# Performance work log

Hardware: AMD Instinct MI355X
Metric: run time of the kernel (lower is better)

Reference implementation:

```python
import jax, jax.numpy as jnp
import numpy as np

B, K, D_MODEL = 64, 256, 512
D_STATE, D_CONV, EXPAND = 16, 4, 1
D_INNER = EXPAND * D_MODEL
DT_RANK = (D_MODEL + 15) // 16  # 32
EPS = 1e-5


def _layer_norm(x, g, b):
    m = jnp.mean(x, axis=-1, keepdims=True)
    v = jnp.mean(jnp.square(x - m), axis=-1, keepdims=True)
    return (x - m) * jax.lax.rsqrt(v + EPS) * g + b


def _silu(x):
    return x * jax.nn.sigmoid(x)


def _mamba_block(x, in_proj_w, conv_w, conv_b, x_proj_w, dt_proj_w, dt_proj_b, A_log, Dp, out_proj_w):
    # x: (B, K, d_model)
    b, k, _ = x.shape
    d_inner = A_log.shape[0]
    d_state = A_log.shape[1]
    dt_rank = dt_proj_w.shape[1]
    xz = x @ in_proj_w.T                      # (B, K, 2*d_inner)
    xi, z = jnp.split(xz, 2, axis=-1)
    # causal depthwise conv1d, width d_conv
    pad = conv_w.shape[1] - 1
    xp = jnp.pad(xi, ((0, 0), (pad, 0), (0, 0)))
    xc = conv_b + sum(xp[:, w:w + k, :] * conv_w[:, w] for w in range(conv_w.shape[1]))
    xc = _silu(xc)
    proj = xc @ x_proj_w.T                    # (B, K, dt_rank + 2*d_state)
    dtr = proj[..., :dt_rank]
    Bc = proj[..., dt_rank:dt_rank + d_state]  # (B, K, d_state)
    Cc = proj[..., dt_rank + d_state:]         # (B, K, d_state)
    dt = jax.nn.softplus(dtr @ dt_proj_w.T + dt_proj_b)  # (B, K, d_inner)
    A = -jnp.exp(A_log)                       # (d_inner, d_state)

    def step(h, inp):
        dt_t, x_t, B_t, C_t = inp             # (B,d_inner),(B,d_inner),(B,d_state),(B,d_state)
        dA = jnp.exp(dt_t[:, :, None] * A)    # (B, d_inner, d_state)
        h = dA * h + (dt_t * x_t)[:, :, None] * B_t[:, None, :]
        y = jnp.einsum('bds,bs->bd', h, C_t)
        return h, y

    h0 = jnp.zeros((b, d_inner, d_state), x.dtype)
    xs = (dt.transpose(1, 0, 2), xc.transpose(1, 0, 2),
          Bc.transpose(1, 0, 2), Cc.transpose(1, 0, 2))
    _, ys = jax.lax.scan(step, h0, xs)        # ys: (K, B, d_inner)
    y = ys.transpose(1, 0, 2) + xc * Dp       # skip term D*x
    y = y * _silu(z)
    return y @ out_proj_w.T


def setup_inputs() -> dict:
    key = jax.random.key(0)
    ks = jax.random.split(key, 8)
    s = 0.02
    slots = jax.random.normal(ks[0], (B, K, D_MODEL), dtype=jnp.float32)
    in_proj_w = jax.random.normal(ks[1], (2 * D_INNER, D_MODEL), jnp.float32) * s
    conv_w = jax.random.normal(ks[2], (D_INNER, D_CONV), jnp.float32) * 0.1
    conv_b = jnp.zeros((D_INNER,), jnp.float32)
    x_proj_w = jax.random.normal(ks[3], (DT_RANK + 2 * D_STATE, D_INNER), jnp.float32) * s
    dt_proj_w = jax.random.normal(ks[4], (D_INNER, DT_RANK), jnp.float32) * s
    dt_proj_b = jax.random.normal(ks[5], (D_INNER,), jnp.float32) * 0.1 - 4.0  # small softplus(dt)
    A_log = jnp.log(jnp.broadcast_to(jnp.arange(1, D_STATE + 1, dtype=jnp.float32), (D_INNER, D_STATE)))
    Dp = jnp.ones((D_INNER,), jnp.float32)
    out_proj_w = jax.random.normal(ks[6], (D_MODEL, D_INNER), jnp.float32) * s
    ln_g = jnp.ones((D_MODEL,), jnp.float32)
    ln_b = jnp.zeros((D_MODEL,), jnp.float32)
    fln_g = jnp.ones((D_MODEL,), jnp.float32)
    fln_b = jnp.zeros((D_MODEL,), jnp.float32)
    return {"slots": slots, "ln_g": ln_g, "ln_b": ln_b,
            "in_proj_w": in_proj_w, "conv_w": conv_w, "conv_b": conv_b,
            "x_proj_w": x_proj_w, "dt_proj_w": dt_proj_w, "dt_proj_b": dt_proj_b,
            "A_log": A_log, "Dp": Dp, "out_proj_w": out_proj_w,
            "fln_g": fln_g, "fln_b": fln_b}


def reference(slots, ln_g, ln_b, in_proj_w, conv_w, conv_b, x_proj_w,
              dt_proj_w, dt_proj_b, A_log, Dp, out_proj_w, fln_g, fln_b):
    x = slots
    # num_layers = 1: pre-norm -> mamba -> residual
    residual = x
    x = _layer_norm(x, ln_g, ln_b)
    x = _mamba_block(x, in_proj_w, conv_w, conv_b, x_proj_w,
                     dt_proj_w, dt_proj_b, A_log, Dp, out_proj_w)
    x = x + residual
    return _layer_norm(x, fln_g, fln_b)
```

## Files before the change

kernel.cpp:

```cpp
#include <hip/hip_runtime.h>
#include <hip/hip_bf16.h>


#define NTOK 16384
#define DM   512

typedef __attribute__((ext_vector_type(8))) short bf16x8;
typedef __attribute__((ext_vector_type(4))) float f32x4;

__device__ __forceinline__ unsigned short f2bf(float f){
  unsigned int u = __float_as_uint(f);
  u = (u + 0x7fffu + ((u >> 16) & 1u)) >> 16;
  return (unsigned short)u;
}
__device__ __forceinline__ float bfu(unsigned short p){ return __uint_as_float(((unsigned int)p) << 16); }
__device__ __forceinline__ unsigned int pk2(float a, float b){
  return (unsigned int)f2bf(a) | ((unsigned int)f2bf(b) << 16);
}
__device__ __forceinline__ float silu(float a){ return a / (1.f + __expf(-a)); }

__device__ __forceinline__ float qsum(float x){
  x += __int_as_float(__builtin_amdgcn_mov_dpp(__float_as_int(x), 0xB1, 0xF, 0xF, true));
  x += __int_as_float(__builtin_amdgcn_mov_dpp(__float_as_int(x), 0x4E, 0xF, 0xF, true));
  return x;
}

__device__ __forceinline__ void async_cp16(const unsigned short* g, unsigned short* l){
  __builtin_amdgcn_global_load_lds(
      (const __attribute__((address_space(1))) unsigned int*)g,
      (__attribute__((address_space(3))) unsigned int*)l, 16, 0, 0);
}

__global__ __launch_bounds__(256) void k_cvtw(const float* __restrict__ W,
                                              unsigned short* __restrict__ Wb){
  int i = (blockIdx.x*256 + threadIdx.x)*8;
  float4 a = *(const float4*)(W+i);
  float4 b = *(const float4*)(W+i+4);
  uint4 st = { pk2(a.x,a.y), pk2(a.z,a.w), pk2(b.x,b.y), pk2(b.z,b.w) };
  *(uint4*)(Wb+i) = st;
}

__global__ __launch_bounds__(64) void k_ln(const float* __restrict__ x,
                                           const float* __restrict__ g,
                                           const float* __restrict__ b,
                                           unsigned short* __restrict__ out){
  int tok  = blockIdx.x;
  int lane = threadIdx.x;
  const float* row = x + (size_t)tok*DM + lane*8;
  float4 r0 = *(const float4*)row;
  float4 r1 = *(const float4*)(row + 4);
  float v[8] = {r0.x,r0.y,r0.z,r0.w, r1.x,r1.y,r1.z,r1.w};
  float s = 0.f;
  #pragma unroll
  for (int i=0;i<8;i++) s += v[i];
  #pragma unroll
  for (int o=32;o;o>>=1) s += __shfl_xor(s, o, 64);
  float m = s * (1.0f/512.0f);
  float vs = 0.f;
  #pragma unroll
  for (int i=0;i<8;i++){ float d = v[i]-m; vs += d*d; }
  #pragma unroll
  for (int o=32;o;o>>=1) vs += __shfl_xor(vs, o, 64);
  float rs = rsqrtf(vs*(1.0f/512.0f) + 1e-5f);
  float4 g0 = *(const float4*)(g + lane*8);
  float4 g1 = *(const float4*)(g + lane*8 + 4);
  float4 b0 = *(const float4*)(b + lane*8);
  float4 b1 = *(const float4*)(b + lane*8 + 4);
  float gv[8] = {g0.x,g0.y,g0.z,g0.w, g1.x,g1.y,g1.z,g1.w};
  float bv[8] = {b0.x,b0.y,b0.z,b0.w, b1.x,b1.y,b1.z,b1.w};
  float o8[8];
  #pragma unroll
  for (int i=0;i<8;i++) o8[i] = (v[i]-m)*rs*gv[i] + bv[i];
  uint4 st = { pk2(o8[0],o8[1]), pk2(o8[2],o8[3]), pk2(o8[4],o8[5]), pk2(o8[6],o8[7]) };
  *(uint4*)(out + (size_t)tok*DM + lane*8) = st;
}

__global__ __launch_bounds__(256) void k_gemm(const unsigned short* __restrict__ A,
                                              const unsigned short* __restrict__ Wb,
                                              float* __restrict__ out_f,
                                              unsigned short* __restrict__ out_b,
                                              int mode){
  __shared__ unsigned short As[2][128*32];
  __shared__ unsigned short Bs[2][128*32];
  int t0  = blockIdx.x * 128;
  int n0  = blockIdx.y * 128;
  int tid = threadIdx.x;
  int lane = tid & 63;
  int wv  = tid >> 6;
  int mw  = wv & 1, nw = wv >> 1;
  int m15 = lane & 15, quad = lane >> 4;

  int srow   = wv*32 + (lane >> 2);
  int schunk = ((lane & 3) ^ ((lane >> 3) & 3)) * 8;
  const unsigned short* gA = A  + (size_t)(t0 + srow)*DM + schunk;
  const unsigned short* gB = Wb + (size_t)(n0 + srow)*DM + schunk;
  unsigned short* asb0 = &As[0][(wv*32)*32];
  unsigned short* bsb0 = &Bs[0][(wv*32)*32];
  unsigned short* asb1 = &As[1][(wv*32)*32];
  unsigned short* bsb1 = &Bs[1][(wv*32)*32];

  async_cp16(gA,         asb0);
  async_cp16(gA + 16*DM, asb0 + 16*32);
  async_cp16(gB,         bsb0);
  async_cp16(gB + 16*DM, bsb0 + 16*32);

  f32x4 acc[4][4];
  #pragma unroll
  for (int rb=0;rb<4;rb++)
    #pragma unroll
    for (int cb=0;cb<4;cb++) acc[rb][cb] = (f32x4){0.f,0.f,0.f,0.f};

  int rdsw = (quad ^ ((m15 >> 1) & 3)) * 8;
  int cur = 0;
  for (int ks = 0; ks < 16; ks++){
    __syncthreads();
    if (ks < 15){
      const unsigned short* nA = gA + (ks+1)*32;
      const unsigned short* nB = gB + (ks+1)*32;
      unsigned short* na = cur ? asb0 : asb1;
      unsigned short* nb = cur ? bsb0 : bsb1;
      async_cp16(nA,         na);
      async_cp16(nA + 16*DM, na + 16*32);
      async_cp16(nB,         nb);
      async_cp16(nB + 16*DM, nb + 16*32);
    }
    bf16x8 af[4], bfr[4];
    #pragma unroll
    for (int rb=0;rb<4;rb++)
      af[rb] = *(const bf16x8*)&As[cur][(mw*64 + rb*16 + m15)*32 + rdsw];
    #pragma unroll
    for (int cb=0;cb<4;cb++)
      bfr[cb] = *(const bf16x8*)&Bs[cur][(nw*64 + cb*16 + m15)*32 + rdsw];
    #pragma unroll
    for (int rb=0;rb<4;rb++)
      #pragma unroll
      for (int cb=0;cb<4;cb++)
        acc[rb][cb] = __builtin_amdgcn_mfma_f32_16x16x32_bf16(af[rb], bfr[cb], acc[rb][cb], 0, 0, 0);
    cur ^= 1;
  }

  #pragma unroll
  for (int rb=0;rb<4;rb++){
    int tok0 = t0 + mw*64 + rb*16 + quad*4;
    int b    = tok0 >> 8;
    int tl0  = tok0 & 255;
    #pragma unroll
    for (int cb=0;cb<4;cb++){
      int nn = n0 + nw*64 + cb*16 + m15;
      f32x4 v = acc[rb][cb];
      if (mode == 0){
        if (nn < DM){
          *(f32x4*)(out_f + ((size_t)(b*DM + nn))*256 + tl0) = v;
        } else {
          uint2 z2 = { pk2(silu(v[0]), silu(v[1])), pk2(silu(v[2]), silu(v[3])) };
          *(uint2*)(out_b + ((size_t)(b*DM + (nn - DM)))*256 + tl0) = z2;
        }
      } else {
        #pragma unroll
        for (int r=0;r<4;r++) out_f[(size_t)(tok0+r)*DM + nn] = v[r];
      }
    }
  }
}

__global__ __launch_bounds__(256) void k_xproj(const float* __restrict__ xiT,
                                               const float* __restrict__ cw,
                                               const float* __restrict__ cb,
                                               const unsigned short* __restrict__ xpwb,
                                               const unsigned short* __restrict__ dtwb,
                                               const float* __restrict__ dtb,
                                               float* __restrict__ dtT,
                                               float* __restrict__ Bc,
                                               float* __restrict__ Cc){
  __shared__ unsigned short xcb[32*520];
  __shared__ unsigned short Bst[2][64*32];
  __shared__ unsigned short pjA[32*40];
  int t0  = blockIdx.x * 32;
  int b   = t0 >> 8;
  int tl0 = t0 & 255;
  int tid = threadIdx.x;
  int lane = tid & 63;
  int wv  = tid >> 6;
  int m15 = lane & 15, quad = lane >> 4;

  #pragma unroll
  for (int j=0;j<2;j++){
    int d = tid + 256*j;
    float4 cr = *(const float4*)(cw + d*4);
    float a0 = cb[d];
    const float* row = xiT + ((size_t)(b*DM + d))*256;
    float w[36];
    if (tl0 == 0){
      w[0]=w[1]=w[2]=w[3]=0.f;
      #pragma unroll
      for (int q2=0;q2<8;q2++){
        float4 v4 = *(const float4*)(row + q2*4);
        w[4+q2*4]=v4.x; w[5+q2*4]=v4.y; w[6+q2*4]=v4.z; w[7+q2*4]=v4.w;
      }
    } else {
      const float* p4 = row + tl0 - 4;
      #pragma unroll
      for (int q2=0;q2<9;q2++){
        float4 v4 = *(const float4*)(p4 + q2*4);
        w[q2*4]=v4.x; w[1+q2*4]=v4.y; w[2+q2*4]=v4.z; w[3+q2*4]=v4.w;
      }
    }
    #pragma unroll
    for (int t=0;t<32;t++){
      float a = a0 + w[t+1]*cr.x + w[t+2]*cr.y + w[t+3]*cr.z + w[t+4]*cr.w;
      xcb[t*520 + d] = f2bf(silu(a));
    }
  }

  int srow = wv*16 + (lane >> 2);
  int sch  = ((lane & 3) ^ ((lane >> 3) & 3)) * 8;
  async_cp16(xpwb + srow*DM + sch, &Bst[0][(wv*16)*32]);
  __syncthreads();

  int mt = wv & 1, ntp = wv >> 1;
  f32x4 pacc[2];
  pacc[0] = (f32x4){0.f,0.f,0.f,0.f};
  pacc[1] = (f32x4){0.f,0.f,0.f,0.f};
  int rdsw = (quad ^ ((m15 >> 1) & 3)) * 8;
  int cur = 0;
  for (int ks=0; ks<16; ks++){
    if (ks < 15)
      async_cp16(xpwb + srow*DM + (ks+1)*32 + sch, &Bst[cur^1][(wv*16)*32]);
    bf16x8 af = *(const bf16x8*)&xcb[(mt*16 + m15)*520 + ks*32 + quad*8];
    #pragma unroll
    for (int j2=0;j2<2;j2++){
      int nt = ntp*2 + j2;
      bf16x8 bfr = *(const bf16x8*)&Bst[cur][(nt*16 + m15)*32 + rdsw];
      pacc[j2] = __builtin_amdgcn_mfma_f32_16x16x32_bf16(af, bfr, pacc[j2], 0, 0, 0);
    }
    cur ^= 1;
    __syncthreads();
  }

  if (ntp == 0){
    #pragma unroll
    for (int j2=0;j2<2;j2++){
      int col = j2*16 + m15;
      #pragma unroll
      for (int r=0;r<4;r++)
        pjA[(mt*16 + quad*4 + r)*40 + col] = f2bf(pacc[j2][r]);
    }
  } else {
    #pragma unroll
    for (int j2=0;j2<2;j2++){
      int c = j2*16 + m15;
      #pragma unroll
      for (int r=0;r<4;r++){
        int tt = t0 + mt*16 + quad*4 + r;
        float v = pacc[j2][r];
        if (c < 16) Bc[(size_t)tt*16 + c] = v;
        else        Cc[(size_t)tt*16 + (c-16)] = v;
      }
    }
  }
  __syncthreads();

  bf16x8 adt = *(const bf16x8*)&pjA[(mt*16 + m15)*40 + quad*8];
  int nh = wv >> 1;
  #pragma unroll
  for (int j2=0;j2<16;j2++){
    int nn = (nh*16 + j2)*16 + m15;
    bf16x8 bfr = *(const bf16x8*)(dtwb + nn*32 + quad*8);
    f32x4 dacc = (f32x4){0.f,0.f,0.f,0.f};
    dacc = __builtin_amdgcn_mfma_f32_16x16x32_bf16(adt, bfr, dacc, 0, 0, 0);
    float bb = dtb[nn];
    f32x4 o;
    #pragma unroll
    for (int r=0;r<4;r++){
      float s = dacc[r] + bb;
      o[r] = (s > 20.f) ? s : log1pf(__expf(s));
    }
    *(f32x4*)(dtT + ((size_t)(b*DM + nn))*256 + tl0 + mt*16 + quad*4) = o;
  }
}

#define SCAN_STEP(DV, XT, BV, CV, ZS, OUT) do {                                 \
    float a_ = fmaf((XT),cr.w, fmaf(xm1,cr.z, fmaf(xm2,cr.y, fmaf(xm3,cr.x, cbv)))); \
    float u_ = a_ / (1.f + __expf(-a_));                                        \
    float dv_ = (DV);                                                           \
    float du_ = dv_*u_;                                                         \
    h0 = fmaf(exp2f(dv_*A0), h0, du_*(BV).x);                                   \
    h1 = fmaf(exp2f(dv_*A1), h1, du_*(BV).y);                                   \
    h2 = fmaf(exp2f(dv_*A2), h2, du_*(BV).z);                                   \
    h3 = fmaf(exp2f(dv_*A3), h3, du_*(BV).w);                                   \
    float yy_ = fmaf(h3,(CV).w, fmaf(h2,(CV).z, fmaf(h1,(CV).y, h0*(CV).x)));   \
    yy_ = qsum(yy_);                                                            \
    OUT = fmaf(u_, Dv, yy_) * (ZS);                                             \
    xm3 = xm2; xm2 = xm1; xm1 = (XT);                                           \
  } while(0)

#define SCAN_LOAD(DT4, XI4, ZZ, B0,B1,B2,B3, C0,C1,C2,C3) do {                  \
    DT4 = *(const float4*)dtp;  XI4 = *(const float4*)xip;                      \
    ZZ  = *(const uint2*)zsp;                                                   \
    B0 = *(const float4*)(Bp);    B1 = *(const float4*)(Bp+16);                 \
    B2 = *(const float4*)(Bp+32); B3 = *(const float4*)(Bp+48);                 \
    C0 = *(const float4*)(Cp);    C1 = *(const float4*)(Cp+16);                 \
    C2 = *(const float4*)(Cp+32); C3 = *(const float4*)(Cp+48);                 \
    dtp += 4; xip += 4; zsp += 4; Bp += 64; Cp += 64;                           \
  } while(0)

#define SCAN_BODY(DT4, XI4, ZZ, B0,B1,B2,B3, C0,C1,C2,C3) do {                  \
    float zs0_ = __uint_as_float((ZZ).x << 16);                                 \
    float zs1_ = __uint_as_float((ZZ).x & 0xffff0000u);                         \
    float zs2_ = __uint_as_float((ZZ).y << 16);                                 \
    float zs3_ = __uint_as_float((ZZ).y & 0xffff0000u);                         \
    float o0_,o1_,o2_,o3_;                                                      \
    SCAN_STEP((DT4).x,(XI4).x,B0,C0,zs0_,o0_);                                  \
    SCAN_STEP((DT4).y,(XI4).y,B1,C1,zs1_,o1_);                                  \
    SCAN_STEP((DT4).z,(XI4).z,B2,C2,zs2_,o2_);                                  \
    SCAN_STEP((DT4).w,(XI4).w,B3,C3,zs3_,o3_);                                  \
    float osel_ = (sl==0)?o0_:(sl==1)?o1_:(sl==2)?o2_:o3_;                      \
    *yo = f2bf(osel_);                                                          \
    yo += 4*DM;                                                                 \
  } while(0)

__global__ __launch_bounds__(256) void k_scan(const float* __restrict__ dtT,
                                              const float* __restrict__ xiT,
                                              const unsigned short* __restrict__ zsT,
                                              const float* __restrict__ Bc,
                                              const float* __restrict__ Cc,
                                              const float* __restrict__ cw,
                                              const float* __restrict__ cb,
                                              const float* __restrict__ Alog,
                                              const float* __restrict__ Dpw,
                                              unsigned short* __restrict__ ya){
  int tid = threadIdx.x;
  int sl  = tid & 3;
  int q   = blockIdx.x*64 + (tid >> 2);
  int d   = q & 511;
  int b   = q >> 9;
  const float LOG2E = 1.44269504f;
  float4 Alr = *(const float4*)(Alog + d*16 + sl*4);
  float A0 = -__expf(Alr.x)*LOG2E, A1 = -__expf(Alr.y)*LOG2E;
  float A2 = -__expf(Alr.z)*LOG2E, A3 = -__expf(Alr.w)*LOG2E;
  float Dv = Dpw[d];
  float4 cr = *(const float4*)(cw + d*4);
  float cbv = cb[d];
  float h0=0.f, h1=0.f, h2=0.f, h3=0.f;
  float xm1=0.f, xm2=0.f, xm3=0.f;
  const float* dtp = dtT + (size_t)q*256;
  const float* xip = xiT + (size_t)q*256;
  const unsigned short* zsp = zsT + (size_t)q*256;
  unsigned short* yo = ya + (size_t)b*256*DM + d + sl*DM;
  const float* Bp = Bc + (size_t)b*4096 + sl*4;
  const float* Cp = Cc + (size_t)b*4096 + sl*4;

  float4 dtA, xiA, a0,a1,a2,a3, e0,e1,e2,e3; uint2 zzA;
  float4 dtB, xiB, f0,f1,f2,f3, g0,g1,g2,g3; uint2 zzB;

  SCAN_LOAD(dtA,xiA,zzA, a0,a1,a2,a3, e0,e1,e2,e3);
  for (int it = 0; it < 64; it += 2){
    SCAN_LOAD(dtB,xiB,zzB, f0,f1,f2,f3, g0,g1,g2,g3);
    SCAN_BODY(dtA,xiA,zzA, a0,a1,a2,a3, e0,e1,e2,e3);
    if (it < 62)
      SCAN_LOAD(dtA,xiA,zzA, a0,a1,a2,a3, e0,e1,e2,e3);
    SCAN_BODY(dtB,xiB,zzB, f0,f1,f2,f3, g0,g1,g2,g3);
  }
}

__global__ __launch_bounds__(64) void k_fln(const float* __restrict__ o,
                                            const float* __restrict__ resid,
                                            const float* __restrict__ g,
                                            const float* __restrict__ b,
                                            float* __restrict__ out){
  int tok  = blockIdx.x;
  int lane = threadIdx.x;
  const float* row = o     + (size_t)tok*DM + lane*8;
  const float* rr  = resid + (size_t)tok*DM + lane*8;
  float4 r0 = *(const float4*)row;
  float4 r1 = *(const float4*)(row + 4);
  float4 s0 = *(const float4*)rr;
  float4 s1 = *(const float4*)(rr + 4);
  float v[8] = {r0.x+s0.x, r0.y+s0.y, r0.z+s0.z, r0.w+s0.w,
                r1.x+s1.x, r1.y+s1.y, r1.z+s1.z, r1.w+s1.w};
  float s = 0.f;
  #pragma unroll
  for (int i=0;i<8;i++) s += v[i];
  #pragma unroll
  for (int o2=32;o2;o2>>=1) s += __shfl_xor(s, o2, 64);
  float m = s * (1.0f/512.0f);
  float vs = 0.f;
  #pragma unroll
  for (int i=0;i<8;i++){ float d = v[i]-m; vs += d*d; }
  #pragma unroll
  for (int o2=32;o2;o2>>=1) vs += __shfl_xor(vs, o2, 64);
  float rs = rsqrtf(vs*(1.0f/512.0f) + 1e-5f);
  float4 g0 = *(const float4*)(g + lane*8);
  float4 g1 = *(const float4*)(g + lane*8 + 4);
  float4 b0 = *(const float4*)(b + lane*8);
  float4 b1 = *(const float4*)(b + lane*8 + 4);
  float gv[8] = {g0.x,g0.y,g0.z,g0.w, g1.x,g1.y,g1.z,g1.w};
  float bv[8] = {b0.x,b0.y,b0.z,b0.w, b1.x,b1.y,b1.z,b1.w};
  float o8[8];
  #pragma unroll
  for (int i=0;i<8;i++) o8[i] = (v[i]-m)*rs*gv[i] + bv[i];
  float4* op = (float4*)(out + (size_t)tok*DM + lane*8);
  op[0] = make_float4(o8[0],o8[1],o8[2],o8[3]);
  op[1] = make_float4(o8[4],o8[5],o8[6],o8[7]);
}

extern "C" void kernel_launch(void* const* d_in, const int* in_sizes, int n_in,
                              void* d_out, int out_size, void* d_ws, size_t ws_size,
                              hipStream_t stream) {
  const float* slots     = (const float*)d_in[0];
  const float* ln_g      = (const float*)d_in[1];
  const float* ln_b      = (const float*)d_in[2];
  const float* in_proj_w = (const float*)d_in[3];
  const float* conv_w    = (const float*)d_in[4];
  const float* conv_b    = (const float*)d_in[5];
  const float* x_proj_w  = (const float*)d_in[6];
  const float* dt_proj_w = (const float*)d_in[7];
  const float* dt_proj_b = (const float*)d_in[8];
  const float* A_log     = (const float*)d_in[9];
  const float* Dp        = (const float*)d_in[10];
  const float* out_projw = (const float*)d_in[11];
  const float* fln_g     = (const float*)d_in[12];
  const float* fln_b     = (const float*)d_in[13];
  float* out = (float*)d_out;

  const size_t MB = 1024*1024;
  char* base = (char*)d_ws;
  float*          xiT  = (float*)(base);
  unsigned short* xlnb = (unsigned short*)(base + 32*MB);
  unsigned short* yab  = xlnb;
  unsigned short* xpwb = xlnb;
  unsigned short* dtwb = xlnb + 32768;
  unsigned short* zsT  = (unsigned short*)(base + 48*MB);
  unsigned short* WbO  = zsT;
  float*          dto  = (float*)(base + 64*MB);
  unsigned short* WbI  = (unsigned short*)dto;
  float*          Bc   = (float*)(base + 96*MB);
  float*          Cc   = (float*)(base + 97*MB);

  k_ln   <<<NTOK,           64, 0, stream>>>(slots, ln_g, ln_b, xlnb);
  k_cvtw <<<256,           256, 0, stream>>>(in_proj_w, WbI);
  k_gemm <<<dim3(128, 8),  256, 0, stream>>>(xlnb, WbI, xiT, zsT, 0);
  k_cvtw <<<16,            256, 0, stream>>>(x_proj_w, xpwb);
  k_cvtw <<<8,             256, 0, stream>>>(dt_proj_w, dtwb);
  k_xproj<<<NTOK/32,       256, 0, stream>>>(xiT, conv_w, conv_b, xpwb, dtwb, dt_proj_b,
                                             dto, Bc, Cc);
  k_scan <<<512,           256, 0, stream>>>(dto, xiT, zsT, Bc, Cc, conv_w, conv_b, A_log, Dp, yab);
  k_cvtw <<<128,           256, 0, stream>>>(out_projw, WbO);
  k_gemm <<<dim3(128, 4),  256, 0, stream>>>(yab, WbO, dto, (unsigned short*)0, 1);
  k_fln  <<<NTOK,           64, 0, stream>>>(dto, slots, fln_g, fln_b, out);
}
```

Measured before the change: 301.6 us.

## Store dt and conv output as bf16 so scan stops recomputing conv

The xproj kernel now writes the post-SiLU conv output transposed in bf16 and stores dt in bf16 instead of fp32. The scan kernel reads these directly, so it no longer recomputes the causal conv and SiLU, and it moves half as many bytes for dt and x. The cost is an extra transposed write in xproj and lower precision for dt and u in the recurrence, which could affect accuracy.

```diff
diff --git a/kernel.cpp b/kernel.cpp
--- a/kernel.cpp
+++ b/kernel.cpp
@@ -169,7 +169,8 @@
                                                const unsigned short* __restrict__ xpwb,
                                                const unsigned short* __restrict__ dtwb,
                                                const float* __restrict__ dtb,
-                                               float* __restrict__ dtT,
+                                               unsigned short* __restrict__ dtTb,
+                                               unsigned short* __restrict__ xcT,
                                                float* __restrict__ Bc,
                                                float* __restrict__ Cc){
   __shared__ unsigned short xcb[32*520];
@@ -205,11 +206,22 @@
         w[q2*4]=v4.x; w[1+q2*4]=v4.y; w[2+q2*4]=v4.z; w[3+q2*4]=v4.w;
       }
     }
+    unsigned short us[32];
     #pragma unroll
     for (int t=0;t<32;t++){
       float a = a0 + w[t+1]*cr.x + w[t+2]*cr.y + w[t+3]*cr.z + w[t+4]*cr.w;
-      xcb[t*520 + d] = f2bf(silu(a));
-    }
+      us[t] = f2bf(silu(a));
+      xcb[t*520 + d] = us[t];
+    }
+    unsigned int pk[16];
+    #pragma unroll
+    for (int t=0;t<16;t++)
+      pk[t] = (unsigned int)us[2*t] | ((unsigned int)us[2*t+1] << 16);
+    uint4* xr = (uint4*)(xcT + ((size_t)(b*DM + d))*256 + tl0);
+    xr[0] = *(uint4*)&pk[0];
+    xr[1] = *(uint4*)&pk[4];
+    xr[2] = *(uint4*)&pk[8];
+    xr[3] = *(uint4*)&pk[12];
   }
 
   int srow = wv*16 + (lane >> 2);
@@ -269,20 +281,20 @@
     f32x4 dacc = (f32x4){0.f,0.f,0.f,0.f};
     dacc = __builtin_amdgcn_mfma_f32_16x16x32_bf16(adt, bfr, dacc, 0, 0, 0);
     float bb = dtb[nn];
-    f32x4 o;
+    float o[4];
     #pragma unroll
     for (int r=0;r<4;r++){
       float s = dacc[r] + bb;
       o[r] = (s > 20.f) ? s : log1pf(__expf(s));
     }
-    *(f32x4*)(dtT + ((size_t)(b*DM + nn))*256 + tl0 + mt*16 + quad*4) = o;
-  }
-}
-
-#define SCAN_STEP(DV, XT, BV, CV, ZS, OUT) do {                                 \
-    float a_ = fmaf((XT),cr.w, fmaf(xm1,cr.z, fmaf(xm2,cr.y, fmaf(xm3,cr.x, cbv)))); \
-    float u_ = a_ / (1.f + __expf(-a_));                                        \
+    uint2 dst = { pk2(o[0],o[1]), pk2(o[2],o[3]) };
+    *(uint2*)(dtTb + ((size_t)(b*DM + nn))*256 + tl0 + mt*16 + quad*4) = dst;
+  }
+}
+
+#define SCAN_STEP(DV, UV, BV, CV, ZS, OUT) do {                                 \
     float dv_ = (DV);                                                           \
+    float u_  = (UV);                                                           \
     float du_ = dv_*u_;                                                         \
     h0 = fmaf(exp2f(dv_*A0), h0, du_*(BV).x);                                   \
     h1 = fmaf(exp2f(dv_*A1), h1, du_*(BV).y);                                   \
@@ -291,41 +303,46 @@
     float yy_ = fmaf(h3,(CV).w, fmaf(h2,(CV).z, fmaf(h1,(CV).y, h0*(CV).x)));   \
     yy_ = qsum(yy_);                                                            \
     OUT = fmaf(u_, Dv, yy_) * (ZS);                                             \
-    xm3 = xm2; xm2 = xm1; xm1 = (XT);                                           \
   } while(0)
 
-#define SCAN_LOAD(DT4, XI4, ZZ, B0,B1,B2,B3, C0,C1,C2,C3) do {                  \
-    DT4 = *(const float4*)dtp;  XI4 = *(const float4*)xip;                      \
+#define SCAN_LOAD(DD, UU, ZZ, B0,B1,B2,B3, C0,C1,C2,C3) do {                    \
+    DD  = *(const uint2*)dtp;  UU = *(const uint2*)xup;                         \
     ZZ  = *(const uint2*)zsp;                                                   \
     B0 = *(const float4*)(Bp);    B1 = *(const float4*)(Bp+16);                 \
     B2 = *(const float4*)(Bp+32); B3 = *(const float4*)(Bp+48);                 \
     C0 = *(const float4*)(Cp);    C1 = *(const float4*)(Cp+16);                 \
     C2 = *(const float4*)(Cp+32); C3 = *(const float4*)(Cp+48);                 \
-    dtp += 4; xip += 4; zsp += 4; Bp += 64; Cp += 64;                           \
+    dtp += 4; xup += 4; zsp += 4; Bp += 64; Cp += 64;                           \
   } while(0)
 
-#define SCAN_BODY(DT4, XI4, ZZ, B0,B1,B2,B3, C0,C1,C2,C3) do {                  \
+#define SCAN_BODY(DD, UU, ZZ, B0,B1,B2,B3, C0,C1,C2,C3) do {                    \
+    float dv0_ = __uint_as_float((DD).x << 16);                                 \
+    float dv1_ = __uint_as_float((DD).x & 0xffff0000u);                         \
+    float dv2_ = __uint_as_float((DD).y << 16);                                 \
+    float dv3_ = __uint_as_float((DD).y & 0xffff0000u);                         \
+    float u0_ = __uint_as_float((UU).x << 16);                                  \
+    float u1_ = __uint_as_float((UU).x & 0xffff0000u);                          \
+    float u2_ = __uint_as_float((UU).y << 16);                                  \
+    float u3_ = __uint_as_float((UU).y & 0xffff0000u);                          \
     float zs0_ = __uint_as_float((ZZ).x << 16);                                 \
     float zs1_ = __uint_as_float((ZZ).x & 0xffff0000u);                         \
     float zs2_ = __uint_as_float((ZZ).y << 16);                                 \
     float zs3_ = __uint_as_float((ZZ).y & 0xffff0000u);                         \
     float o0_,o1_,o2_,o3_;                                                      \
-    SCAN_STEP((DT4).x,(XI4).x,B0,C0,zs0_,o0_);                                  \
-    SCAN_STEP((DT4).y,(XI4).y,B1,C1,zs1_,o1_);                                  \
-    SCAN_STEP((DT4).z,(XI4).z,B2,C2,zs2_,o2_);                                  \
-    SCAN_STEP((DT4).w,(XI4).w,B3,C3,zs3_,o3_);                                  \
+    SCAN_STEP(dv0_,u0_,B0,C0,zs0_,o0_);                                         \
+    SCAN_STEP(dv1_,u1_,B1,C1,zs1_,o1_);                                         \
+    SCAN_STEP(dv2_,u2_,B2,C2,zs2_,o2_);                                         \
+    SCAN_STEP(dv3_,u3_,B3,C3,zs3_,o3_);                                         \
     float osel_ = (sl==0)?o0_:(sl==1)?o1_:(sl==2)?o2_:o3_;                      \
     *yo = f2bf(osel_);                                                          \
     yo += 4*DM;                                                                 \
   } while(0)
 
-__global__ __launch_bounds__(256) void k_scan(const float* __restrict__ dtT,
-                                              const float* __restrict__ xiT,
+__global__ __launch_bounds__(256) void k_scan(const unsigned short* __restrict__ dtT,
+                                              const unsigned short* __restrict__ xcT,
                                               const unsigned short* __restrict__ zsT,
                                               const float* __restrict__ Bc,
                                               const float* __restrict__ Cc,
-                                              const float* __restrict__ cw,
-                                              const float* __restrict__ cb,
                                               const float* __restrict__ Alog,
                                               const float* __restrict__ Dpw,
                                               unsigned short* __restrict__ ya){
@@ -339,27 +356,24 @@
   float A0 = -__expf(Alr.x)*LOG2E, A1 = -__expf(Alr.y)*LOG2E;
   float A2 = -__expf(Alr.z)*LOG2E, A3 = -__expf(Alr.w)*LOG2E;
   float Dv = Dpw[d];
-  float4 cr = *(const float4*)(cw + d*4);
-  float cbv = cb[d];
   float h0=0.f, h1=0.f, h2=0.f, h3=0.f;
-  float xm1=0.f, xm2=0.f, xm3=0.f;
-  const float* dtp = dtT + (size_t)q*256;
-  const float* xip = xiT + (size_t)q*256;
+  const unsigned short* dtp = dtT + (size_t)q*256;
+  const unsigned short* xup = xcT + (size_t)q*256;
   const unsigned short* zsp = zsT + (size_t)q*256;
   unsigned short* yo = ya + (size_t)b*256*DM + d + sl*DM;
   const float* Bp = Bc + (size_t)b*4096 + sl*4;
   const float* Cp = Cc + (size_t)b*4096 + sl*4;
 
-  float4 dtA, xiA, a0,a1,a2,a3, e0,e1,e2,e3; uint2 zzA;
-  float4 dtB, xiB, f0,f1,f2,f3, g0,g1,g2,g3; uint2 zzB;
-
-  SCAN_LOAD(dtA,xiA,zzA, a0,a1,a2,a3, e0,e1,e2,e3);
+  uint2 ddA, uuA, zzA; float4 a0,a1,a2,a3, e0,e1,e2,e3;
+  uint2 ddB, uuB, zzB; float4 f0,f1,f2,f3, g0,g1,g2,g3;
+
+  SCAN_LOAD(ddA,uuA,zzA, a0,a1,a2,a3, e0,e1,e2,e3);
   for (int it = 0; it < 64; it += 2){
-    SCAN_LOAD(dtB,xiB,zzB, f0,f1,f2,f3, g0,g1,g2,g3);
-    SCAN_BODY(dtA,xiA,zzA, a0,a1,a2,a3, e0,e1,e2,e3);
+    SCAN_LOAD(ddB,uuB,zzB, f0,f1,f2,f3, g0,g1,g2,g3);
+    SCAN_BODY(ddA,uuA,zzA, a0,a1,a2,a3, e0,e1,e2,e3);
     if (it < 62)
-      SCAN_LOAD(dtA,xiA,zzA, a0,a1,a2,a3, e0,e1,e2,e3);
-    SCAN_BODY(dtB,xiB,zzB, f0,f1,f2,f3, g0,g1,g2,g3);
+      SCAN_LOAD(ddA,uuA,zzA, a0,a1,a2,a3, e0,e1,e2,e3);
+    SCAN_BODY(ddB,uuB,zzB, f0,f1,f2,f3, g0,g1,g2,g3);
   }
 }
 
@@ -432,6 +446,8 @@
   unsigned short* dtwb = xlnb + 32768;
   unsigned short* zsT  = (unsigned short*)(base + 48*MB);
   unsigned short* WbO  = zsT;
+  unsigned short* dtTb = (unsigned short*)(base + 64*MB);
+  unsigned short* xcT  = (unsigned short*)(base + 80*MB);
   float*          dto  = (float*)(base + 64*MB);
   unsigned short* WbI  = (unsigned short*)dto;
   float*          Bc   = (float*)(base + 96*MB);
@@ -443,8 +459,8 @@
   k_cvtw <<<16,            256, 0, stream>>>(x_proj_w, xpwb);
   k_cvtw <<<8,             256, 0, stream>>>(dt_proj_w, dtwb);
   k_xproj<<<NTOK/32,       256, 0, stream>>>(xiT, conv_w, conv_b, xpwb, dtwb, dt_proj_b,
-                                             dto, Bc, Cc);
-  k_scan <<<512,           256, 0, stream>>>(dto, xiT, zsT, Bc, Cc, conv_w, conv_b, A_log, Dp, yab);
+                                             dtTb, xcT, Bc, Cc);
+  k_scan <<<512,           256, 0, stream>>>(dtTb, xcT, zsT, Bc, Cc, A_log, Dp, yab);
   k_cvtw <<<128,           256, 0, stream>>>(out_projw, WbO);
   k_gemm <<<dim3(128, 4),  256, 0, stream>>>(yab, WbO, dto, (unsigned short*)0, 1);
   k_fln  <<<NTOK,           64, 0, stream>>>(dto, slots, fln_g, fln_b, out);
```

New measurement: 299.1 us. About the same (-0.8%).
